# Kernel optimization log

Measured on AMD Instinct MI355X. Metric: run time of the kernel, lower is better.

The kernel has to match this reference:

```python
import jax, jax.numpy as jnp
import numpy as np
import math

B, S, D = 2, 4096, 1024
H, HD = 16, 64
R = 16

def _rope(x, cos, sin):
    # x: [B, S, H, HD]; cos/sin: [S, HD//2]
    xr = x.reshape(*x.shape[:-1], HD // 2, 2)
    xe, xo = xr[..., 0], xr[..., 1]
    c = cos[None, :, None, :]
    s = sin[None, :, None, :]
    # complex multiply (xe + i*xo) * (c + i*s)
    re = xe * c - xo * s
    im = xe * s + xo * c
    return jnp.stack([re, im], axis=-1).reshape(x.shape)

def setup_inputs() -> dict:
    key = jax.random.key(0)
    ks = jax.random.split(key, 20)
    inp = {}
    inp["x"] = jax.random.normal(ks[0], (B, S, D), dtype=jnp.float32)
    pos = jnp.arange(S, dtype=jnp.float32)
    inv_freq = 1.0 / (10000.0 ** (jnp.arange(0, HD, 2, dtype=jnp.float32) / HD))
    ang = pos[:, None] * inv_freq[None, :]  # [S, HD//2]
    inp["freqs_cos"] = jnp.cos(ang)
    inp["freqs_sin"] = jnp.sin(ang)
    causal = jnp.triu(jnp.full((S, S), -1e9, dtype=jnp.float32), k=1)
    inp["mask"] = causal[None, None, :, :]
    sc = 1.0 / math.sqrt(D)
    inp["wq_w"] = jax.random.normal(ks[1], (D, D), dtype=jnp.float32) * sc
    inp["wq_b"] = jnp.zeros((D,), dtype=jnp.float32)
    inp["wk_w"] = jax.random.normal(ks[2], (D, D), dtype=jnp.float32) * sc
    inp["wv_w"] = jax.random.normal(ks[3], (D, D), dtype=jnp.float32) * sc
    inp["wo_w"] = jax.random.normal(ks[4], (D, D), dtype=jnp.float32) * sc
    inp["wo_b"] = jnp.zeros((D,), dtype=jnp.float32)
    for i, nm in enumerate(["q", "k", "v", "o"]):
        inp[f"lora_{nm}_l1"] = jax.random.normal(ks[5 + 2 * i], (R, D), dtype=jnp.float32) * sc
        inp[f"lora_{nm}_l2"] = jax.random.normal(ks[6 + 2 * i], (D, R), dtype=jnp.float32) * 0.01
    return inp

def reference(x, freqs_cos, freqs_sin, mask, wq_w, wq_b, wk_w, wv_w, wo_w, wo_b,
              lora_q_l1, lora_q_l2, lora_k_l1, lora_k_l2,
              lora_v_l1, lora_v_l2, lora_o_l1, lora_o_l2):
    # QKV projections + LoRA deltas (torch Linear: y = x @ W.T + b, W is [out, in])
    xq = x @ wq_w.T + wq_b + (x @ lora_q_l1.T) @ lora_q_l2.T
    xk = x @ wk_w.T + (x @ lora_k_l1.T) @ lora_k_l2.T
    xv = x @ wv_w.T + (x @ lora_v_l1.T) @ lora_v_l2.T
    xq = xq.reshape(B, S, H, HD)
    xk = xk.reshape(B, S, H, HD)
    xv = xv.reshape(B, S, H, HD)
    xq = _rope(xq, freqs_cos, freqs_sin)
    xk = _rope(xk, freqs_cos, freqs_sin)
    # attention (training path: keys/values = current xk/xv, causal mask additive)
    scores = jnp.einsum('bqhd,bkhd->bhqk', xq, xk) / math.sqrt(HD)
    scores = scores + mask
    probs = jax.nn.softmax(scores.astype(jnp.float32), axis=-1).astype(xq.dtype)
    out = jnp.einsum('bhqk,bkhd->bqhd', probs, xv).reshape(B, S, D)
    return out @ wo_w.T + wo_b + (out @ lora_o_l1.T) @ lora_o_l2.T
```

## Files before the change

### kernel.cpp

```cpp
#include <hip/hip_runtime.h>
#include <hip/hip_bf16.h>
#include <stdint.h>

#define S_DIM 4096
#define D_DIM 1024
#define M_ROWS 8192

typedef short bf16x8 __attribute__((ext_vector_type(8)));
typedef float f32x4  __attribute__((ext_vector_type(4)));

__device__ __forceinline__ f32x4 mfma16(bf16x8 a, bf16x8 b, f32x4 c) {
  return __builtin_amdgcn_mfma_f32_16x16x32_bf16(a, b, c, 0, 0, 0);
}
__device__ __forceinline__ short f2bs(float f) {
  __hip_bfloat16 h = __float2bfloat16(f);
  return *reinterpret_cast<short*>(&h);
}
__device__ __forceinline__ short f2bs_fast(float f) {
  unsigned u = __builtin_bit_cast(unsigned, f) + 0x8000u;
  return (short)(u >> 16);
}
__device__ __forceinline__ unsigned pk2bf(float a, float b) {
  unsigned ua = __builtin_bit_cast(unsigned, a) + 0x8000u;
  unsigned ub = __builtin_bit_cast(unsigned, b) + 0x8000u;
  return __builtin_amdgcn_perm(ub, ua, 0x07060302);
}
__device__ __forceinline__ float fexp2(float x) {
  return __builtin_amdgcn_exp2f(x);
}
__device__ __forceinline__ void gload16(const void* g, void* l) {
  __builtin_amdgcn_global_load_lds(
      (const __attribute__((address_space(1))) unsigned int*)g,
      (__attribute__((address_space(3))) unsigned int*)l, 16, 0, 0);
}

__global__ void prep_k(const float* __restrict__ x,
                       const float* __restrict__ wq, const float* __restrict__ wk,
                       const float* __restrict__ wv, const float* __restrict__ wo,
                       const float* __restrict__ wqb,
                       const float* __restrict__ lq1, const float* __restrict__ lq2,
                       const float* __restrict__ lk1, const float* __restrict__ lk2,
                       const float* __restrict__ lv1, const float* __restrict__ lv2,
                       const float* __restrict__ lo1, const float* __restrict__ lo2,
                       const float* __restrict__ cf, const float* __restrict__ sf,
                       short* __restrict__ xaug, short* __restrict__ wqkv,
                       short* __restrict__ woeff,
                       float* __restrict__ biasc, float* __restrict__ cs2)
{
  unsigned i = blockIdx.x * 256u + threadIdx.x;
  if (i < 8388608u) {
    xaug[i] = f2bs(x[i]);
    return;
  }
  i -= 8388608u;
  if (i < 3145728u) {
    unsigned n = i >> 10, k = i & 1023u;
    const float *wsrc, *l1, *l2;
    unsigned nn;
    if (n < 1024u)      { wsrc = wq; l1 = lq1; l2 = lq2; nn = n; }
    else if (n < 2048u) { wsrc = wk; l1 = lk1; l2 = lk2; nn = n - 1024u; }
    else                { wsrc = wv; l1 = lv1; l2 = lv2; nn = n - 2048u; }
    float v = wsrc[nn * 1024u + k];
#pragma unroll
    for (unsigned r = 0; r < 16u; ++r)
      v += l2[nn * 16u + r] * l1[r * 1024u + k];
    wqkv[i] = f2bs(v);
    return;
  }
  i -= 3145728u;
  if (i < 1048576u) {
    unsigned n = i >> 10, k = i & 1023u;
    float v = wo[i];
#pragma unroll
    for (unsigned r = 0; r < 16u; ++r)
      v += lo2[n * 16u + r] * lo1[r * 1024u + k];
    woeff[i] = f2bs(v);
    return;
  }
  i -= 1048576u;
  if (i < 3072u) {
    biasc[i] = (i < 1024u) ? wqb[i] : 0.f;
    return;
  }
  i -= 3072u;
  if (i < 131072u) {
    cs2[2u * i]     = cf[i];
    cs2[2u * i + 1] = sf[i];
  }
}

template<int MODE>
__global__ __launch_bounds__(256) void gemm_bt(
    const short* __restrict__ A, int lda,
    const short* __restrict__ B, int ldb,
    int N, int K,
    const float* __restrict__ bias,
    void* __restrict__ Cout, int ldc, int colofs,
    short* __restrict__ qo, short* __restrict__ ko, short* __restrict__ vo,
    const float* __restrict__ cs2)
{
  __shared__ short As[2][128 * 32];
  __shared__ short Bs[2][128 * 32];
  const int tid = threadIdx.x;
  const int w = tid >> 6, lane = tid & 63;
  const int q4 = lane >> 4, c = lane & 15;
  const int mh = w >> 1, nh = w & 1;

  const int id = (int)blockIdx.y * gridDim.x + (int)blockIdx.x;
  const int g = id & 7, j = id >> 3;
  const int mt = g * 8 + (j & 7);
  const int nt = j >> 3;

  const int rl = lane >> 2;
  const int kc = (lane & 3) * 8;

  const short* Ag0 = A + (size_t)(mt * 128 + w * 32 + rl) * lda + kc;
  const short* Ag1 = Ag0 + (size_t)16 * lda;
  int rb0 = nt * 128 + w * 32 + rl;      if (rb0 > N - 1) rb0 = N - 1;
  int rb1 = nt * 128 + w * 32 + 16 + rl; if (rb1 > N - 1) rb1 = N - 1;
  const short* Bg0 = B + (size_t)rb0 * ldb + kc;
  const short* Bg1 = B + (size_t)rb1 * ldb + kc;
  const int sD0 = (w * 32) * 32;
  const int sD1 = (w * 32 + 16) * 32;

  f32x4 acc[4][4];
#pragma unroll
  for (int ms = 0; ms < 4; ++ms)
#pragma unroll
    for (int ns = 0; ns < 4; ++ns) acc[ms][ns] = (f32x4){0.f, 0.f, 0.f, 0.f};

  gload16(Ag0, &As[0][sD0]);
  gload16(Ag1, &As[0][sD1]);
  gload16(Bg0, &Bs[0][sD0]);
  gload16(Bg1, &Bs[0][sD1]);
  Ag0 += 32; Ag1 += 32; Bg0 += 32; Bg1 += 32;
  __syncthreads();

  const int nkt = K >> 5;
  for (int kt = 0; kt < nkt; ++kt) {
    const int cur = kt & 1, nxt = cur ^ 1;
    if (kt + 1 < nkt) {
      gload16(Ag0, &As[nxt][sD0]);
      gload16(Ag1, &As[nxt][sD1]);
      gload16(Bg0, &Bs[nxt][sD0]);
      gload16(Bg1, &Bs[nxt][sD1]);
      Ag0 += 32; Ag1 += 32; Bg0 += 32; Bg1 += 32;
    }
    bf16x8 af[4], bfr[4];
#pragma unroll
    for (int ms = 0; ms < 4; ++ms)
      af[ms] = *(const bf16x8*)&As[cur][(mh * 64 + ms * 16 + c) * 32 + q4 * 8];
#pragma unroll
    for (int ns = 0; ns < 4; ++ns)
      bfr[ns] = *(const bf16x8*)&Bs[cur][(nh * 64 + ns * 16 + c) * 32 + q4 * 8];
#pragma unroll
    for (int ms = 0; ms < 4; ++ms)
#pragma unroll
      for (int ns = 0; ns < 4; ++ns)
        acc[ms][ns] = mfma16(af[ms], bfr[ns], acc[ms][ns]);
    __syncthreads();
  }

#pragma unroll
  for (int ms = 0; ms < 4; ++ms) {
#pragma unroll
    for (int ns = 0; ns < 4; ++ns) {
      const int n = nt * 128 + nh * 64 + ns * 16 + c;
      if (MODE == 0) {
        float bsv = (n < N) ? bias[n] : 0.f;
        float* Co = (float*)Cout;
#pragma unroll
        for (int r = 0; r < 4; ++r) {
          int m = mt * 128 + mh * 64 + ms * 16 + q4 * 4 + r;
          if (n < N) Co[(size_t)m * ldc + n] = acc[ms][ns][r] + bsv;
        }
      } else if (MODE == 1) {
        short* Co = (short*)Cout;
#pragma unroll
        for (int r = 0; r < 4; ++r) {
          int m = mt * 128 + mh * 64 + ms * 16 + q4 * 4 + r;
          if (n < N) Co[(size_t)m * ldc + colofs + n] = f2bs_fast(acc[ms][ns][r]);
        }
      } else {
        float bsv = bias[n];
        int which = n >> 10;
        int m0 = mt * 128 + mh * 64 + ms * 16 + q4 * 4;
        int bb = m0 >> 12, spos = m0 & 4095;
        if (which < 2) {
          int h = (n >> 6) & 15;
          int hd = n & 63;
          short* dst = which == 0 ? qo : ko;
          const float sgn = (c & 1) ? 1.f : -1.f;
          const int ihalf = hd >> 1;
#pragma unroll
          for (int r = 0; r < 4; ++r) {
            float val = acc[ms][ns][r] + bsv;
            float part = __shfl_xor(val, 1);
            float2 cs = *(const float2*)&cs2[((size_t)(spos + r) * 32 + ihalf) * 2];
            float res = val * cs.x + part * (sgn * cs.y);
            if (which == 0) res *= 0.18033688011112042f;
            dst[(size_t)((bb * 16 + h) * 4096 + spos + r) * 64 + hd] = f2bs_fast(res);
          }
        } else {
          int h = (n >> 6) & 15;
          int hd = n & 63;
          uint2 vk;
          vk.x = pk2bf(acc[ms][ns][0] + bsv, acc[ms][ns][1] + bsv);
          vk.y = pk2bf(acc[ms][ns][2] + bsv, acc[ms][ns][3] + bsv);
          *(uint2*)&vo[(((size_t)bb * 16 + h) * 64 + hd) * 4096 + spos] = vk;
        }
      }
    }
  }
}

__global__ __launch_bounds__(256, 2) void flash_k(
    const short* __restrict__ Qb, const short* __restrict__ Kb,
    const short* __restrict__ Vt, short* __restrict__ Oaug)
{
  __shared__ short lds[24576];
  short* const PL = &lds[16384];

  const int id = (int)blockIdx.y * 16 + (int)blockIdx.x;
  const int g = id & 7, j = id >> 3;
  const int bh = g * 4 + (j >> 4);
  const int bx = j & 15;

  const int tid = threadIdx.x;
  const int w = tid >> 6, lane = tid & 63;
  const int q4 = lane >> 4, c = lane & 15;

  const short* Kg = Kb + (size_t)bh * 4096 * 64;
  const short* Vg = Vt + (size_t)bh * 64 * 4096;

  const int l8 = lane >> 3, l7 = lane & 7;
  const int sw = (l7 ^ l8) * 8;
  const int G0 = w * 2, G1 = w * 2 + 1;
  const int koff0 = (G0 * 8 + l8) * 64 + sw;
  const int koff1 = (G1 * 8 + l8) * 64 + sw;
  const int voff0 = (G0 * 8 + l8) * 4096 + sw;
  const int voff1 = (G1 * 8 + l8) * 4096 + sw;
  const int qg = w * 4;
  const int qoff0 = ((qg + 0) * 8 + l8) * 64 + sw;
  const int qoff1 = ((qg + 1) * 8 + l8) * 64 + sw;
  const int qoff2 = ((qg + 2) * 8 + l8) * 64 + sw;
  const int qoff3 = ((qg + 3) * 8 + l8) * 64 + sw;

  const int c7 = c & 7;
  const int chA0 = ((q4) ^ c7) * 8;
  const int chA1 = ((4 + q4) ^ c7) * 8;
  const int rowc = c * 64;
  const int rowq = (w * 16 + c) * 64;
  const int pw_base = (w * 16 + c) * 64 + (q4 & 1) * 4;
  const int pw_g = q4 >> 1;

  const int b = bh >> 4, h = bh & 15;

  for (int half = 0; half < 2; ++half) {
    const int qt = half == 0 ? 31 - bx : bx;
    const short* Qg = Qb + ((size_t)bh * 4096 + qt * 128) * 64;

    gload16(Qg + qoff0, &lds[16384 + (qg + 0) * 512]);
    gload16(Qg + qoff1, &lds[16384 + (qg + 1) * 512]);
    gload16(Qg + qoff2, &lds[16384 + (qg + 2) * 512]);
    gload16(Qg + qoff3, &lds[16384 + (qg + 3) * 512]);
    gload16(Kg + koff0, &lds[G0 * 512]);
    gload16(Kg + koff1, &lds[G1 * 512]);
    gload16(Vg + voff0, &lds[8192 + G0 * 512]);
    gload16(Vg + voff1, &lds[8192 + G1 * 512]);
    __syncthreads();

    bf16x8 qa0 = *(const bf16x8*)(PL + rowq + chA0);
    bf16x8 qa1 = *(const bf16x8*)(PL + rowq + chA1);
    bf16x8 qb0 = *(const bf16x8*)(PL + 4096 + rowq + chA0);
    bf16x8 qb1 = *(const bf16x8*)(PL + 4096 + rowq + chA1);

    f32x4 oa[4], ob[4];
#pragma unroll
    for (int i = 0; i < 4; ++i) {
      oa[i] = (f32x4){0.f, 0.f, 0.f, 0.f};
      ob[i] = (f32x4){0.f, 0.f, 0.f, 0.f};
    }
    float la = 0.f, lb = 0.f;

    const int last = 2 * qt + 1;
    for (int kt = 0; kt <= last; ++kt) {
      const int cur = (kt & 1) * 4096;
      const short* Kc = &lds[cur];
      const short* Vc = &lds[8192 + cur];
      if (kt < last) {
        const int nxt = ((kt + 1) & 1) * 4096;
        const short* ks = Kg + (size_t)(kt + 1) * 4096;
        const short* vs = Vg + (size_t)(kt + 1) * 64;
        gload16(ks + koff0, &lds[nxt + G0 * 512]);
        gload16(ks + koff1, &lds[nxt + G1 * 512]);
        gload16(vs + voff0, &lds[8192 + nxt + G0 * 512]);
        gload16(vs + voff1, &lds[8192 + nxt + G1 * 512]);
      }
      const bool doA = (kt <= 2 * qt);

      f32x4 sa[4], sb[4];
#pragma unroll
      for (int ns = 0; ns < 4; ++ns) {
        bf16x8 kf0 = *(const bf16x8*)(Kc + ns * 1024 + rowc + chA0);
        bf16x8 kf1 = *(const bf16x8*)(Kc + ns * 1024 + rowc + chA1);
        sa[ns] = mfma16(kf0, qa0, (f32x4){0.f, 0.f, 0.f, 0.f});
        sa[ns] = mfma16(kf1, qa1, sa[ns]);
        sb[ns] = mfma16(kf0, qb0, (f32x4){0.f, 0.f, 0.f, 0.f});
        sb[ns] = mfma16(kf1, qb1, sb[ns]);
      }
      if (kt == 2 * qt) {
#pragma unroll
        for (int ns = 0; ns < 4; ++ns)
#pragma unroll
          for (int r = 0; r < 4; ++r)
            if (ns * 16 + q4 * 4 + r > w * 16 + c) sa[ns][r] = -1e30f;
      }
      if (kt == last) {
#pragma unroll
        for (int ns = 0; ns < 4; ++ns)
#pragma unroll
          for (int r = 0; r < 4; ++r)
            if (ns * 16 + q4 * 4 + r > w * 16 + c) sb[ns][r] = -1e30f;
      }

      bf16x8 pfa0, pfa1;
      if (doA) {
        float ps[4][4];
#pragma unroll
        for (int ns = 0; ns < 4; ++ns)
#pragma unroll
          for (int r = 0; r < 4; ++r) ps[ns][r] = fexp2(sa[ns][r]);
        float s0 = (ps[0][0] + ps[0][1]) + (ps[0][2] + ps[0][3]);
        float s1 = (ps[1][0] + ps[1][1]) + (ps[1][2] + ps[1][3]);
        float s2 = (ps[2][0] + ps[2][1]) + (ps[2][2] + ps[2][3]);
        float s3 = (ps[3][0] + ps[3][1]) + (ps[3][2] + ps[3][3]);
        float sum = (s0 + s1) + (s2 + s3);
        sum += __shfl_xor(sum, 16);
        sum += __shfl_xor(sum, 32);
        la += sum;
#pragma unroll
        for (int ns = 0; ns < 4; ++ns) {
          uint2 pk;
          pk.x = pk2bf(ps[ns][0], ps[ns][1]);
          pk.y = pk2bf(ps[ns][2], ps[ns][3]);
          *(uint2*)(PL + pw_base + (((ns * 2 + pw_g) ^ c7) * 8)) = pk;
        }
        pfa0 = *(const bf16x8*)(PL + rowq + chA0);
        pfa1 = *(const bf16x8*)(PL + rowq + chA1);
      }
      {
        float ps[4][4];
#pragma unroll
        for (int ns = 0; ns < 4; ++ns)
#pragma unroll
          for (int r = 0; r < 4; ++r) ps[ns][r] = fexp2(sb[ns][r]);
        float s0 = (ps[0][0] + ps[0][1]) + (ps[0][2] + ps[0][3]);
        float s1 = (ps[1][0] + ps[1][1]) + (ps[1][2] + ps[1][3]);
        float s2 = (ps[2][0] + ps[2][1]) + (ps[2][2] + ps[2][3]);
        float s3 = (ps[3][0] + ps[3][1]) + (ps[3][2] + ps[3][3]);
        float sum = (s0 + s1) + (s2 + s3);
        sum += __shfl_xor(sum, 16);
        sum += __shfl_xor(sum, 32);
        lb += sum;
#pragma unroll
        for (int ns = 0; ns < 4; ++ns) {
          uint2 pk;
          pk.x = pk2bf(ps[ns][0], ps[ns][1]);
          pk.y = pk2bf(ps[ns][2], ps[ns][3]);
          *(uint2*)(PL + 4096 + pw_base + (((ns * 2 + pw_g) ^ c7) * 8)) = pk;
        }
      }
      bf16x8 pfb0 = *(const bf16x8*)(PL + 4096 + rowq + chA0);
      bf16x8 pfb1 = *(const bf16x8*)(PL + 4096 + rowq + chA1);

#pragma unroll
      for (int nc = 0; nc < 4; ++nc) {
        bf16x8 vf0 = *(const bf16x8*)(Vc + nc * 1024 + rowc + chA0);
        bf16x8 vf1 = *(const bf16x8*)(Vc + nc * 1024 + rowc + chA1);
        if (doA) {
          oa[nc] = mfma16(vf0, pfa0, oa[nc]);
          oa[nc] = mfma16(vf1, pfa1, oa[nc]);
        }
        ob[nc] = mfma16(vf0, pfb0, ob[nc]);
        ob[nc] = mfma16(vf1, pfb1, ob[nc]);
      }
      __syncthreads();
    }

    float lia = 1.f / la, lib = 1.f / lb;
#pragma unroll
    for (int nc = 0; nc < 4; ++nc) {
      uint2 ok;
      ok.x = pk2bf(oa[nc][0] * lia, oa[nc][1] * lia);
      ok.y = pk2bf(oa[nc][2] * lia, oa[nc][3] * lia);
      *(uint2*)(PL + pw_base + (((nc * 2 + pw_g) ^ c7) * 8)) = ok;
      uint2 ok2;
      ok2.x = pk2bf(ob[nc][0] * lib, ob[nc][1] * lib);
      ok2.y = pk2bf(ob[nc][2] * lib, ob[nc][3] * lib);
      *(uint2*)(PL + 4096 + pw_base + (((nc * 2 + pw_g) ^ c7) * 8)) = ok2;
    }
    __syncthreads();
#pragma unroll
    for (int i2 = 0; i2 < 4; ++i2) {
      int ch = tid + i2 * 256;
      int r = ch >> 3, g2 = ch & 7;
      size_t row = (size_t)b * 4096 + qt * 128 + r;
      *(int4*)&Oaug[row * 1024 + h * 64 + g2 * 8] =
          *(const int4*)(PL + r * 64 + ((g2 ^ (r & 7)) * 8));
    }
    __syncthreads();
  }
}

extern "C" void kernel_launch(void* const* d_in, const int* in_sizes, int n_in,
                              void* d_out, int out_size, void* d_ws, size_t ws_size,
                              hipStream_t stream) {
  const float* x   = (const float*)d_in[0];
  const float* fc  = (const float*)d_in[1];
  const float* fs  = (const float*)d_in[2];
  const float* wq  = (const float*)d_in[4];
  const float* wqb = (const float*)d_in[5];
  const float* wk  = (const float*)d_in[6];
  const float* wv  = (const float*)d_in[7];
  const float* wo  = (const float*)d_in[8];
  const float* wob = (const float*)d_in[9];
  const float* lq1 = (const float*)d_in[10];
  const float* lq2 = (const float*)d_in[11];
  const float* lk1 = (const float*)d_in[12];
  const float* lk2 = (const float*)d_in[13];
  const float* lv1 = (const float*)d_in[14];
  const float* lv2 = (const float*)d_in[15];
  const float* lo1 = (const float*)d_in[16];
  const float* lo2 = (const float*)d_in[17];

  char* ws = (char*)d_ws;
  const size_t OFF_XAUG  = 0;
  const size_t OFF_XOAUG = 16777216;
  const size_t OFF_WQKV  = 33554432;
  const size_t OFF_WOEFF = 39845888;
  const size_t OFF_BIASC = 41943040;
  const size_t OFF_QB    = 41955328;
  const size_t OFF_KB    = 58732544;
  const size_t OFF_VT    = 75509760;
  const size_t OFF_CS    = 92286976;

  short* xaug  = (short*)(ws + OFF_XAUG);
  short* xoaug = (short*)(ws + OFF_XOAUG);
  short* wqkv  = (short*)(ws + OFF_WQKV);
  short* woeff = (short*)(ws + OFF_WOEFF);
  float* biasc = (float*)(ws + OFF_BIASC);
  short* qb    = (short*)(ws + OFF_QB);
  short* kb    = (short*)(ws + OFF_KB);
  short* vt    = (short*)(ws + OFF_VT);
  float* cs2   = (float*)(ws + OFF_CS);

  prep_k<<<49676, 256, 0, stream>>>(x, wq, wk, wv, wo, wqb,
                                    lq1, lq2, lk1, lk2, lv1, lv2, lo1, lo2,
                                    fc, fs,
                                    xaug, wqkv, woeff, biasc, cs2);
  gemm_bt<2><<<dim3(24, 64), 256, 0, stream>>>(xaug, 1024, wqkv, 1024, 3072, 1024,
                                               biasc, nullptr, 0, 0, qb, kb, vt,
                                               cs2);
  flash_k<<<dim3(16, 32), 256, 0, stream>>>(qb, kb, vt, xoaug);
  gemm_bt<0><<<dim3(8, 64), 256, 0, stream>>>(xoaug, 1024, woeff, 1024, 1024, 1024,
                                              wob, d_out, 1024, 0,
                                              nullptr, nullptr, nullptr, nullptr);
}
```

Baseline: 365.4 us.

## Double GEMM K-tile to 64 with XOR-swizzled LDS layout

Raises the GEMM K tile from 32 to 64 so each barrier-separated iteration issues twice the MFMAs, halving the synchronisation count. The LDS layout gets an XOR swizzle on 16-byte chunks to avoid bank conflicts on the wider rows. LDS use doubles, and the clamp on B row indices for partial N tiles is dropped, which risks out-of-bounds reads when N is not a multiple of 128.

```diff
diff --git a/kernel.cpp b/kernel.cpp
--- a/kernel.cpp
+++ b/kernel.cpp
@@ -99,8 +99,8 @@
     short* __restrict__ qo, short* __restrict__ ko, short* __restrict__ vo,
     const float* __restrict__ cs2)
 {
-  __shared__ short As[2][128 * 32];
-  __shared__ short Bs[2][128 * 32];
+  __shared__ short As[2][128 * 64];
+  __shared__ short Bs[2][128 * 64];
   const int tid = threadIdx.x;
   const int w = tid >> 6, lane = tid & 63;
   const int q4 = lane >> 4, c = lane & 15;
@@ -111,17 +111,17 @@
   const int mt = g * 8 + (j & 7);
   const int nt = j >> 3;
 
-  const int rl = lane >> 2;
-  const int kc = (lane & 3) * 8;
-
-  const short* Ag0 = A + (size_t)(mt * 128 + w * 32 + rl) * lda + kc;
-  const short* Ag1 = Ag0 + (size_t)16 * lda;
-  int rb0 = nt * 128 + w * 32 + rl;      if (rb0 > N - 1) rb0 = N - 1;
-  int rb1 = nt * 128 + w * 32 + 16 + rl; if (rb1 > N - 1) rb1 = N - 1;
-  const short* Bg0 = B + (size_t)rb0 * ldb + kc;
-  const short* Bg1 = B + (size_t)rb1 * ldb + kc;
-  const int sD0 = (w * 32) * 32;
-  const int sD1 = (w * 32 + 16) * 32;
+  const int l8 = lane >> 3, l7 = lane & 7;
+  const int sw = (l7 ^ l8) * 8;
+  const int c7 = c & 7;
+  const short* Ags[4];
+  const short* Bgs[4];
+#pragma unroll
+  for (int t = 0; t < 4; ++t) {
+    Ags[t] = A + (size_t)(mt * 128 + (w * 4 + t) * 8 + l8) * lda + sw;
+    Bgs[t] = B + (size_t)(nt * 128 + (w * 4 + t) * 8 + l8) * ldb + sw;
+  }
+  const int sDb = (w * 4) * 512;
 
   f32x4 acc[4][4];
 #pragma unroll
@@ -129,35 +129,41 @@
 #pragma unroll
     for (int ns = 0; ns < 4; ++ns) acc[ms][ns] = (f32x4){0.f, 0.f, 0.f, 0.f};
 
-  gload16(Ag0, &As[0][sD0]);
-  gload16(Ag1, &As[0][sD1]);
-  gload16(Bg0, &Bs[0][sD0]);
-  gload16(Bg1, &Bs[0][sD1]);
-  Ag0 += 32; Ag1 += 32; Bg0 += 32; Bg1 += 32;
+#pragma unroll
+  for (int t = 0; t < 4; ++t) {
+    gload16(Ags[t], &As[0][sDb + t * 512]);
+    gload16(Bgs[t], &Bs[0][sDb + t * 512]);
+    Ags[t] += 64; Bgs[t] += 64;
+  }
   __syncthreads();
 
-  const int nkt = K >> 5;
+  const int nkt = K >> 6;
   for (int kt = 0; kt < nkt; ++kt) {
     const int cur = kt & 1, nxt = cur ^ 1;
     if (kt + 1 < nkt) {
-      gload16(Ag0, &As[nxt][sD0]);
-      gload16(Ag1, &As[nxt][sD1]);
-      gload16(Bg0, &Bs[nxt][sD0]);
-      gload16(Bg1, &Bs[nxt][sD1]);
-      Ag0 += 32; Ag1 += 32; Bg0 += 32; Bg1 += 32;
-    }
-    bf16x8 af[4], bfr[4];
-#pragma unroll
-    for (int ms = 0; ms < 4; ++ms)
-      af[ms] = *(const bf16x8*)&As[cur][(mh * 64 + ms * 16 + c) * 32 + q4 * 8];
-#pragma unroll
-    for (int ns = 0; ns < 4; ++ns)
-      bfr[ns] = *(const bf16x8*)&Bs[cur][(nh * 64 + ns * 16 + c) * 32 + q4 * 8];
-#pragma unroll
-    for (int ms = 0; ms < 4; ++ms)
+#pragma unroll
+      for (int t = 0; t < 4; ++t) {
+        gload16(Ags[t], &As[nxt][sDb + t * 512]);
+        gload16(Bgs[t], &Bs[nxt][sDb + t * 512]);
+        Ags[t] += 64; Bgs[t] += 64;
+      }
+    }
+#pragma unroll
+    for (int s = 0; s < 2; ++s) {
+      const int ch = ((s * 4 + q4) ^ c7) * 8;
+      bf16x8 af[4], bfr[4];
+#pragma unroll
+      for (int ms = 0; ms < 4; ++ms)
+        af[ms] = *(const bf16x8*)&As[cur][(mh * 64 + ms * 16 + c) * 64 + ch];
 #pragma unroll
       for (int ns = 0; ns < 4; ++ns)
-        acc[ms][ns] = mfma16(af[ms], bfr[ns], acc[ms][ns]);
+        bfr[ns] = *(const bf16x8*)&Bs[cur][(nh * 64 + ns * 16 + c) * 64 + ch];
+#pragma unroll
+      for (int ms = 0; ms < 4; ++ms)
+#pragma unroll
+        for (int ns = 0; ns < 4; ++ns)
+          acc[ms][ns] = mfma16(af[ms], bfr[ns], acc[ms][ns]);
+    }
     __syncthreads();
   }
 
```

Result: no change. 367.1 us (+0.5%).
